# Performance work log

Hardware: AMD Instinct MI355X
Metric: run time of the kernel (lower is better)

The kernel has to match this reference:

```python
import jax, jax.numpy as jnp
import numpy as np
from jax import lax

RULE_START = 85
ALPHA = 0.2
SIGMA = 0.05


def setup_inputs() -> dict:
    key = jax.random.key(0)
    ks = jax.random.split(key, 10)
    T, B, H, NR, NO = 512, 256, 512, 20, 33
    D = RULE_START + NR
    s = lambda fan_in: 1.0 / np.sqrt(fan_in)
    return {
        "x": jax.random.normal(ks[0], (T, B, D), jnp.float32),
        "noise": jax.random.uniform(ks[1], (T, B, H), jnp.float32),
        "Ws_w": jax.random.normal(ks[2], (H, RULE_START), jnp.float32) * s(RULE_START),
        "Ws_b": jax.random.normal(ks[3], (H,), jnp.float32) * s(RULE_START),
        "Wr_w": jax.random.normal(ks[4], (H, NR), jnp.float32) * s(NR),
        "Wrec_w": jax.random.normal(ks[5], (H, H), jnp.float32) * s(H),
        "Wrec_b": jax.random.normal(ks[6], (H,), jnp.float32) * s(H),
        "mask": jnp.ones((H, H), jnp.float32),
        "Wout_w": jax.random.normal(ks[7], (NO, H), jnp.float32) * s(H),
        "Wout_b": jax.random.normal(ks[8], (NO,), jnp.float32) * s(H),
    }


def reference(x, noise, Ws_w, Ws_b, Wr_w, Wrec_w, Wrec_b, mask, Wout_w, Wout_b):
    # x: [T, B, rule_start + n_rule]
    sensory = x[:, :, :RULE_START]
    rule = x[:, :, RULE_START:]
    # input projections, batched over all T*B at once
    rnn_inputs = (jnp.einsum('tbd,hd->tbh', sensory, Ws_w) + Ws_b
                  + jnp.einsum('tbr,hr->tbh', rule, Wr_w))  # [T, B, H]
    masked_w = Wrec_w * mask  # [H, H]
    rec_noise = noise * SIGMA  # [T, B, H]

    h0 = jnp.zeros(rnn_inputs.shape[1:], rnn_inputs.dtype)  # [B, H]

    def step(h, inp):
        inp_t, noise_t = inp
        out = jax.nn.relu(inp_t + noise_t + h @ masked_w.T + Wrec_b)
        h_new = ALPHA * out + (1.0 - ALPHA) * h
        return h_new, h_new

    _, hidden_states = lax.scan(step, h0, (rnn_inputs, rec_noise))  # [T, B, H]
    out = jnp.einsum('tbh,oh->tbo', hidden_states, Wout_w) + Wout_b  # [T, B, n_output]
    return out
```

## Files before the change

kernel.cpp:

```cpp
#include <hip/hip_runtime.h>

#define TT 512
#define BB 256
#define HH 512
#define DD 105
#define RS 85
#define NRULE 20
#define NOUT 33
#define HALF 256

#define NFRAG_REC 512
#define NFRAG_IN  128
#define NFRAG_OUT 48
#define FRAG_IN_OFF  (NFRAG_REC)
#define FRAG_OUT_OFF (NFRAG_REC + NFRAG_IN)
#define NFRAG_TOT (NFRAG_REC + NFRAG_IN + NFRAG_OUT)

#define WP_BYTES    ((size_t)NFRAG_TOT * 1024)

#define PREC_OFF    WP_BYTES
#define PREC_STRIDE ((size_t)32768)
#define POUT_OFF    (PREC_OFF + 32 * PREC_STRIDE)
#define POUT_STRIDE ((size_t)9216)
#define EXCH_BYTES  (32 * PREC_STRIDE + 16 * POUT_STRIDE)

#define BPRE_OFF    WP_BYTES
#define BPRE_BYTES  ((size_t)TT * 16 * 16 * 512 * 2)
#define SNEED       (BPRE_OFF + BPRE_BYTES)

#define RETRY_GUARD 100000

typedef __bf16 bf16x8 __attribute__((ext_vector_type(8)));
typedef float  f32x4  __attribute__((ext_vector_type(4)));
typedef unsigned long long u64;
typedef unsigned short us;

__device__ __forceinline__ us f2bf(float f) {
  unsigned u = __builtin_bit_cast(unsigned, f);
  u += 0x7FFFu + ((u >> 16) & 1u);
  return (us)(u >> 16);
}
__device__ __forceinline__ float bf2f(us v) {
  return __builtin_bit_cast(float, (unsigned)v << 16);
}
__device__ __forceinline__ u64 ld_agent(const u64* p) {
  return __hip_atomic_load(p, __ATOMIC_RELAXED, __HIP_MEMORY_SCOPE_AGENT);
}
__device__ __forceinline__ void st_agent(u64* p, u64 v) {
  __hip_atomic_store(p, v, __ATOMIC_RELAXED, __HIP_MEMORY_SCOPE_AGENT);
}
__device__ __forceinline__ float bfhi(unsigned w) {
  return __builtin_bit_cast(float, w & 0xffff0000u);
}
__device__ __forceinline__ unsigned pkv(float v, unsigned tag) {
  return ((unsigned)f2bf(v) << 16) | tag;
}
__device__ __forceinline__ int tags4_ok(u64 v0, u64 v1, u64 v2, u64 v3, unsigned tag) {
  return (((unsigned)v0 & 0xffffu) == tag) & (((unsigned)(v0 >> 32) & 0xffffu) == tag)
       & (((unsigned)v1 & 0xffffu) == tag) & (((unsigned)(v1 >> 32) & 0xffffu) == tag)
       & (((unsigned)v2 & 0xffffu) == tag) & (((unsigned)(v2 >> 32) & 0xffffu) == tag)
       & (((unsigned)v3 & 0xffffu) == tag) & (((unsigned)(v3 >> 32) & 0xffffu) == tag);
}
__device__ __forceinline__ int tags2_ok(u64 v0, u64 v1, unsigned tag) {
  return (((unsigned)v0 & 0xffffu) == tag) & (((unsigned)(v0 >> 32) & 0xffffu) == tag)
       & (((unsigned)v1 & 0xffffu) == tag) & (((unsigned)(v1 >> 32) & 0xffffu) == tag);
}

__global__ void pack_weights(const float* __restrict__ Ws_w, const float* __restrict__ Wr_w,
                             const float* __restrict__ Wrec_w, const float* __restrict__ mask,
                             const float* __restrict__ Wout_w, us* __restrict__ wp)
{
  int gid = blockIdx.x * blockDim.x + threadIdx.x;
  if (gid >= NFRAG_TOT * 64) return;
  int f = gid >> 6, lane = gid & 63;
  int m16 = lane & 15, kg = lane >> 4;
  float v[8];
  if (f < NFRAG_REC) {
    int mt = f >> 4, kt = f & 15;
    int m = mt * 16 + m16, k0 = kt * 32 + kg * 8;
#pragma unroll
    for (int j = 0; j < 8; ++j) {
      int k = k0 + j;
      v[j] = Wrec_w[m * HH + k] * mask[m * HH + k];
    }
  } else if (f < FRAG_OUT_OFF) {
    int ff = f - FRAG_IN_OFF;
    int mt = ff >> 2, kt = ff & 3;
    int m = mt * 16 + m16, k0 = kt * 32 + kg * 8;
#pragma unroll
    for (int j = 0; j < 8; ++j) {
      int k = k0 + j;
      float val = 0.f;
      if (k < RS) val = Ws_w[m * RS + k];
      else if (k < DD) val = Wr_w[m * NRULE + (k - RS)];
      v[j] = val;
    }
  } else {
    int ff = f - FRAG_OUT_OFF;
    int mt = ff >> 4, kt = ff & 15;
    int m = mt * 16 + m16, k0 = kt * 32 + kg * 8;
#pragma unroll
    for (int j = 0; j < 8; ++j) {
      int k = k0 + j;
      v[j] = (m < NOUT) ? Wout_w[m * HH + k] : 0.f;
    }
  }
  unsigned o[4];
#pragma unroll
  for (int j = 0; j < 4; ++j)
    o[j] = (unsigned)f2bf(v[2 * j]) | ((unsigned)f2bf(v[2 * j + 1]) << 16);
  uint4 st = make_uint4(o[0], o[1], o[2], o[3]);
  *reinterpret_cast<uint4*>(wp + (size_t)f * 512 + lane * 8) = st;
}

__global__ __launch_bounds__(512)
void precompute_pre(const float* __restrict__ x, const float* __restrict__ noise,
                    const float* __restrict__ Ws_b, const float* __restrict__ Wrec_b,
                    const us* __restrict__ wp, us* __restrict__ pre)
{
  __shared__ alignas(16) us x_lds[16 * 128];
  const int t  = blockIdx.x >> 4;
  const int gg = blockIdx.x & 15;
  const int gb = gg * 16;
  const int tid = threadIdx.x;
  const int wv = tid >> 6, lane = tid & 63;
  const int bcol = lane & 15, krow = lane >> 4;
  const int sw = (bcol & 7) << 3;
  const uint4* wp4 = reinterpret_cast<const uint4*>(wp);

  for (int i = tid; i < 16 * 128; i += 512) x_lds[i] = 0;
  __syncthreads();
  if (tid < 420) {
    f32x4 xv = reinterpret_cast<const f32x4*>(x + ((size_t)t * BB + gb) * DD)[tid];
#pragma unroll
    for (int j = 0; j < 4; ++j) {
      int e = tid * 4 + j;
      int b = e / DD, k = e - b * DD;
      x_lds[b * 128 + (k ^ ((b & 7) << 3))] = f2bf(xv[j]);
    }
  }
  __syncthreads();

  us ov[16];
#pragma unroll
  for (int jj = 0; jj < 4; ++jj) {
    int m = wv * 4 + jj;
    f32x4 acc = {0.f, 0.f, 0.f, 0.f};
#pragma unroll
    for (int kx = 0; kx < 4; ++kx) {
      int k0 = kx * 32 + krow * 8;
      bf16x8 xb = __builtin_bit_cast(bf16x8,
          *reinterpret_cast<const uint4*>(&x_lds[bcol * 128 + (k0 ^ sw)]));
      bf16x8 aw = __builtin_bit_cast(bf16x8, wp4[(FRAG_IN_OFF + m * 4 + kx) * 64 + lane]);
      acc = __builtin_amdgcn_mfma_f32_16x16x32_bf16(aw, xb, acc, 0, 0, 0);
    }
    int h0 = m * 16 + krow * 4;
    f32x4 b1 = *reinterpret_cast<const f32x4*>(Ws_b + h0);
    f32x4 b2 = *reinterpret_cast<const f32x4*>(Wrec_b + h0);
    f32x4 nz = *reinterpret_cast<const f32x4*>(noise + ((size_t)t * BB + gb + bcol) * HH + h0);
#pragma unroll
    for (int r = 0; r < 4; ++r)
      ov[jj * 4 + r] = f2bf(acc[r] + b1[r] + b2[r] + 0.05f * nz[r]);
  }
  us* dst = pre + (((size_t)t * 16 + gg) * 512 + tid) * 16;
  *reinterpret_cast<uint4*>(dst)     = *reinterpret_cast<uint4*>(&ov[0]);
  *reinterpret_cast<uint4*>(dst + 8) = *reinterpret_cast<uint4*>(&ov[8]);
}

__global__ __launch_bounds__(512, 2)
void rnn_seq16(unsigned char* __restrict__ ws)
{
  __shared__ alignas(16) us h_lds[2][16 * 512];
  __shared__ alignas(16) us wlds[112 * 512];

  const int tid  = threadIdx.x;
  const int wv   = tid >> 6;
  const int lane = tid & 63;
  const int bcol = lane & 15;
  const int krow = lane >> 4;
  const int g    = blockIdx.x;
  const int sw   = (bcol & 7) << 3;
  const uint4* wp4 = reinterpret_cast<const uint4*>(ws);
  us* pre = (us*)(ws + BPRE_OFF);

  {
    us* hz = &h_lds[0][0];
    for (int i = tid; i < 2 * 16 * 512; i += 512) hz[i] = 0;
  }
  for (int c = tid; c < 112 * 64; c += 512) {
    int fl = c >> 6, l = c & 63;
    int w = fl / 14, kt = fl % 14;
    int mt = 4 * w + 3;
    uint4 v = wp4[(mt * 16 + kt) * 64 + l];
    *reinterpret_cast<uint4*>(&wlds[fl * 512 + l * 8]) = v;
  }

  bf16x8 wreg[3][16];
#pragma unroll
  for (int j = 0; j < 3; ++j)
#pragma unroll
    for (int kt = 0; kt < 16; ++kt)
      wreg[j][kt] = __builtin_bit_cast(bf16x8, wp4[((4 * wv + j) * 16 + kt) * 64 + lane]);
  bf16x8 wx[2];
#pragma unroll
  for (int j = 0; j < 2; ++j)
    wx[j] = __builtin_bit_cast(bf16x8, wp4[((4 * wv + 3) * 16 + 14 + j) * 64 + lane]);

  int h0[4];
#pragma unroll
  for (int j = 0; j < 4; ++j) h0[j] = (4 * wv + j) * 16 + krow * 4;

  __syncthreads();

  const size_t tstride = (size_t)16 * 512 * 16;
  us* pio = pre + ((size_t)g * 512 + tid) * 16;

  uint4 hs[2] = {};

#pragma unroll 1
  for (int t = 0; t < TT; ++t) {
    const int cur = t & 1;
    if (t > 0) {
      us* hout = pio + (size_t)(t - 1) * tstride;
      *reinterpret_cast<uint4*>(hout)     = hs[0];
      *reinterpret_cast<uint4*>(hout + 8) = hs[1];
    }
    uint4 pA[2];
    {
      const us* pn = pio + (size_t)t * tstride;
      pA[0] = *reinterpret_cast<const uint4*>(pn);
      pA[1] = *reinterpret_cast<const uint4*>(pn + 8);
    }

    f32x4 acc[4];
#pragma unroll
    for (int j = 0; j < 4; ++j) acc[j] = f32x4{0.f, 0.f, 0.f, 0.f};
    __builtin_amdgcn_s_setprio(1);
#pragma unroll
    for (int kt = 0; kt < 16; ++kt) {
      bf16x8 hb = __builtin_bit_cast(bf16x8,
          *reinterpret_cast<const uint4*>(&h_lds[cur][bcol * 512 + ((kt * 32 + krow * 8) ^ sw)]));
      acc[0] = __builtin_amdgcn_mfma_f32_16x16x32_bf16(wreg[0][kt], hb, acc[0], 0, 0, 0);
      acc[1] = __builtin_amdgcn_mfma_f32_16x16x32_bf16(wreg[1][kt], hb, acc[1], 0, 0, 0);
      acc[2] = __builtin_amdgcn_mfma_f32_16x16x32_bf16(wreg[2][kt], hb, acc[2], 0, 0, 0);
      bf16x8 wl;
      if (kt < 14)
        wl = __builtin_bit_cast(bf16x8,
            *reinterpret_cast<const uint4*>(&wlds[(wv * 14 + kt) * 512 + lane * 8]));
      else
        wl = wx[kt - 14];
      acc[3] = __builtin_amdgcn_mfma_f32_16x16x32_bf16(wl, hb, acc[3], 0, 0, 0);
    }
    __builtin_amdgcn_s_setprio(0);

    {
      const us* pa = reinterpret_cast<const us*>(pA);
      us* hh = reinterpret_cast<us*>(hs);
#pragma unroll
      for (int j = 0; j < 4; ++j)
#pragma unroll
        for (int r = 0; r < 4; ++r) {
          int s = j * 4 + r;
          float v = acc[j][r] + bf2f(pa[s]);
          v = fmaxf(v, 0.f);
          hh[s] = f2bf(0.2f * v + 0.8f * bf2f(hh[s]));
        }
    }
    {
      const us* hh = reinterpret_cast<const us*>(hs);
#pragma unroll
      for (int j = 0; j < 4; ++j) {
        *reinterpret_cast<ushort4*>(&h_lds[cur ^ 1][bcol * 512 + (h0[j] ^ sw)]) =
            make_ushort4(hh[j * 4], hh[j * 4 + 1], hh[j * 4 + 2], hh[j * 4 + 3]);
      }
    }
    __syncthreads();
  }

  {
    us* hout = pio + (size_t)(TT - 1) * tstride;
    *reinterpret_cast<uint4*>(hout)     = hs[0];
    *reinterpret_cast<uint4*>(hout + 8) = hs[1];
  }
}

__global__ __launch_bounds__(256)
void out_gemm(const us* __restrict__ hid, const us* __restrict__ wp,
              const float* __restrict__ Wout_b, float* __restrict__ out)
{
  __shared__ alignas(16) us t_lds[16 * 512];
  const int tid = threadIdx.x;
  const int wv = tid >> 6, lane = tid & 63;
  const int bcol = lane & 15, krow = lane >> 4;
  const int tg = blockIdx.x;
  const int t = tg >> 4, g = tg & 15;
  const int sw = (bcol & 7) << 3;
  const uint4* wp4 = reinterpret_cast<const uint4*>(wp);

#pragma unroll
  for (int q = 0; q < 2; ++q) {
    int cc = tid + q * 256;
    const us* src = hid + (size_t)tg * 8192 + (size_t)cc * 16;
    uint4 v0 = *reinterpret_cast<const uint4*>(src);
    uint4 v1 = *reinterpret_cast<const uint4*>(src + 8);
    us vs[16];
    *reinterpret_cast<uint4*>(&vs[0]) = v0;
    *reinterpret_cast<uint4*>(&vs[8]) = v1;
    int b = cc & 15, kr = (cc >> 4) & 3;
    int swb = (b & 7) << 3;
#pragma unroll
    for (int jj = 0; jj < 4; ++jj) {
      int m = (cc >> 6) * 4 + jj;
      int h = m * 16 + kr * 4;
      *reinterpret_cast<ushort4*>(&t_lds[b * 512 + (h ^ swb)]) =
          make_ushort4(vs[jj * 4], vs[jj * 4 + 1], vs[jj * 4 + 2], vs[jj * 4 + 3]);
    }
  }
  __syncthreads();
  if (wv < 3) {
    f32x4 po = {0.f, 0.f, 0.f, 0.f};
#pragma unroll
    for (int kt = 0; kt < 16; ++kt) {
      bf16x8 hb = __builtin_bit_cast(bf16x8,
          *reinterpret_cast<const uint4*>(&t_lds[bcol * 512 + ((kt * 32 + krow * 8) ^ sw)]));
      bf16x8 ao = __builtin_bit_cast(bf16x8, wp4[(FRAG_OUT_OFF + wv * 16 + kt) * 64 + lane]);
      po = __builtin_amdgcn_mfma_f32_16x16x32_bf16(ao, hb, po, 0, 0, 0);
    }
#pragma unroll
    for (int r = 0; r < 4; ++r) {
      int o = wv * 16 + krow * 4 + r;
      if (o < NOUT)
        out[((size_t)t * BB + g * 16 + bcol) * NOUT + o] = po[r] + Wout_b[o];
    }
  }
}

__global__ __launch_bounds__(512, 2)
void rnn_fused(const float* __restrict__ x, const float* __restrict__ noise,
               const float* __restrict__ Ws_b, const float* __restrict__ Wrec_b,
               const float* __restrict__ Wout_b, unsigned char* __restrict__ ws,
               float* __restrict__ out)
{
  __shared__ alignas(16) us h_lds[16 * HALF];
  __shared__ alignas(16) us x_lds[2][16 * 128];
  __shared__ alignas(16) us win_lds[64 * 512];
  __shared__ alignas(16) us wout_lds[24 * 512];

  const int tid  = threadIdx.x;
  const int wv   = tid >> 6;
  const int lane = tid & 63;
  const int bcol = lane & 15;
  const int krow = lane >> 4;
  const int bid  = blockIdx.x;
  const int g    = bid & 15;
  const int hf   = bid >> 4;
  const int gb   = g * 16;
  const int hbase = hf * HALF;
  const int sw   = (bcol & 7) << 3;
  const bool outduty = (hf == 0);

  const uint4* wp4 = reinterpret_cast<const uint4*>(ws);
  u64* prec_own = (u64*)(ws + PREC_OFF + (size_t)bid * PREC_STRIDE);
  const u64* prec_par = (const u64*)(ws + PREC_OFF + (size_t)(bid ^ 16) * PREC_STRIDE);
  u64* pout_buf = (u64*)(ws + POUT_OFF + (size_t)g * POUT_STRIDE);

  for (int i = tid; i < 16 * HALF; i += 512) h_lds[i] = 0;
  {
    us* xz = &x_lds[0][0];
    for (int i = tid; i < 2 * 16 * 128; i += 512) xz[i] = 0;
  }
  for (int c = tid; c < 64 * 64; c += 512) {
    int fl = c >> 6, l = c & 63;
    uint4 w = wp4[(FRAG_IN_OFF + hf * 64 + fl) * 64 + l];
    *reinterpret_cast<uint4*>(&win_lds[fl * 512 + l * 8]) = w;
  }
  for (int c = tid; c < 24 * 64; c += 512) {
    int fl = c >> 6, l = c & 63;
    int mt_o = fl >> 3, kto = fl & 7;
    uint4 w = wp4[(FRAG_OUT_OFF + mt_o * 16 + hf * 8 + kto) * 64 + l];
    *reinterpret_cast<uint4*>(&wout_lds[fl * 512 + l * 8]) = w;
  }

  bf16x8 wreg_own[2][8], wreg_par[2][8];
#pragma unroll
  for (int j = 0; j < 2; ++j)
#pragma unroll
    for (int kt = 0; kt < 8; ++kt) {
      wreg_own[j][kt] = __builtin_bit_cast(bf16x8,
          wp4[((hf * 16 + 2 * wv + j) * 16 + (hf * 8 + kt)) * 64 + lane]);
      wreg_par[j][kt] = __builtin_bit_cast(bf16x8,
          wp4[(((1 - hf) * 16 + 2 * wv + j) * 16 + (hf * 8 + kt)) * 64 + lane]);
    }

  float bias_reg[2][4];
#pragma unroll
  for (int j = 0; j < 2; ++j)
#pragma unroll
    for (int r = 0; r < 4; ++r) {
      int h = hbase + (2 * wv + j) * 16 + krow * 4 + r;
      bias_reg[j][r] = Ws_b[h] + Wrec_b[h];
    }
  float woutb[4];
#pragma unroll
  for (int r = 0; r < 4; ++r) {
    int o = wv * 16 + krow * 4 + r;
    woutb[r] = (outduty && wv < 3 && o < NOUT) ? Wout_b[o] : 0.f;
  }

  const int rbase = bcol * 256 + 2 * wv * 16 + krow * 4;
  const int ri = rbase >> 1;
  const int oi = (bcol * 48 + wv * 16 + krow * 4) >> 1;

  float hreg[2][4] = {};
  f32x4 nrA[2], nrB[2];
  f32x4 po_hold = {0.f, 0.f, 0.f, 0.f};

  __syncthreads();

  if (tid < 420) {
    f32x4 xv = reinterpret_cast<const f32x4*>(x + (size_t)gb * DD)[tid];
#pragma unroll
    for (int j = 0; j < 4; ++j) {
      int e = tid * 4 + j;
      int b = e / DD, k = e - b * DD;
      x_lds[0][b * 128 + (k ^ ((b & 7) << 3))] = f2bf(xv[j]);
    }
  }
  {
    const float* nb = noise + ((size_t)gb + bcol) * HH + hbase + krow * 4;
#pragma unroll
    for (int j = 0; j < 2; ++j)
      nrA[j] = *reinterpret_cast<const f32x4*>(nb + (2 * wv + j) * 16);
  }
  __syncthreads();

#pragma unroll 1
  for (int t = 0; t < TT; ++t) {
    const int cur = t & 1;
    const unsigned tag = (unsigned)t;
    u64* prec_slot = prec_own + (size_t)(t & 1) * 2048;
    const u64* precp_slot = prec_par + (size_t)(t & 1) * 2048;
    f32x4 xs = {0.f, 0.f, 0.f, 0.f};
    if (t + 1 < TT) {
      if (tid < 420)
        xs = reinterpret_cast<const f32x4*>(x + ((size_t)(t + 1) * BB + gb) * DD)[tid];
      const float* nb = noise + (((size_t)(t + 1)) * BB + gb + bcol) * HH + hbase + krow * 4;
#pragma unroll
      for (int j = 0; j < 2; ++j)
        nrB[j] = *reinterpret_cast<const f32x4*>(nb + (2 * wv + j) * 16);
    }

    if (t > 0) {
      f32x4 pc0 = {0.f,0.f,0.f,0.f}, pc1 = {0.f,0.f,0.f,0.f};
#pragma unroll
      for (int kto = 0; kto < 8; ++kto) {
        int k0 = kto * 32 + krow * 8;
        bf16x8 hb = __builtin_bit_cast(bf16x8,
            *reinterpret_cast<const uint4*>(&h_lds[bcol * HALF + (k0 ^ sw)]));
        pc0 = __builtin_amdgcn_mfma_f32_16x16x32_bf16(wreg_par[0][kto], hb, pc0, 0, 0, 0);
        pc1 = __builtin_amdgcn_mfma_f32_16x16x32_bf16(wreg_par[1][kto], hb, pc1, 0, 0, 0);
      }
      st_agent(prec_slot + ri,     (u64)pkv(pc0[0], tag) | ((u64)pkv(pc0[1], tag) << 32));
      st_agent(prec_slot + ri + 1, (u64)pkv(pc0[2], tag) | ((u64)pkv(pc0[3], tag) << 32));
      st_agent(prec_slot + ri + 8, (u64)pkv(pc1[0], tag) | ((u64)pkv(pc1[1], tag) << 32));
      st_agent(prec_slot + ri + 9, (u64)pkv(pc1[2], tag) | ((u64)pkv(pc1[3], tag) << 32));
    }

    f32x4 acc[2];
    acc[0] = f32x4{0.f,0.f,0.f,0.f};
    acc[1] = f32x4{0.f,0.f,0.f,0.f};
#pragma unroll
    for (int kto = 0; kto < 8; ++kto) {
      int k0 = kto * 32 + krow * 8;
      bf16x8 hb = __builtin_bit_cast(bf16x8,
          *reinterpret_cast<const uint4*>(&h_lds[bcol * HALF + (k0 ^ sw)]));
      acc[0] = __builtin_amdgcn_mfma_f32_16x16x32_bf16(wreg_own[0][kto], hb, acc[0], 0, 0, 0);
      acc[1] = __builtin_amdgcn_mfma_f32_16x16x32_bf16(wreg_own[1][kto], hb, acc[1], 0, 0, 0);
    }
#pragma unroll
    for (int kx = 0; kx < 4; ++kx) {
      int k0 = kx * 32 + krow * 8;
      bf16x8 xb = __builtin_bit_cast(bf16x8,
          *reinterpret_cast<const uint4*>(&x_lds[cur][bcol * 128 + (k0 ^ sw)]));
#pragma unroll
      for (int j = 0; j < 2; ++j) {
        bf16x8 aw = __builtin_bit_cast(bf16x8,
            *reinterpret_cast<const uint4*>(&win_lds[((2 * wv + j) * 4 + kx) * 512 + lane * 8]));
        acc[j] = __builtin_amdgcn_mfma_f32_16x16x32_bf16(aw, xb, acc[j], 0, 0, 0);
      }
    }

    f32x4 po = {0.f, 0.f, 0.f, 0.f};
    if (t > 0 && wv < 3) {
#pragma unroll
      for (int kto = 0; kto < 8; ++kto) {
        int k0 = kto * 32 + krow * 8;
        bf16x8 hb = __builtin_bit_cast(bf16x8,
            *reinterpret_cast<const uint4*>(&h_lds[bcol * HALF + (k0 ^ sw)]));
        bf16x8 ao = __builtin_bit_cast(bf16x8,
            *reinterpret_cast<const uint4*>(&wout_lds[(wv * 8 + kto) * 512 + lane * 8]));
        po = __builtin_amdgcn_mfma_f32_16x16x32_bf16(ao, hb, po, 0, 0, 0);
      }
    }

    f32x4 pa0 = {0.f,0.f,0.f,0.f}, pa1 = {0.f,0.f,0.f,0.f};
    if (t > 0) {
      u64 v0, v1, v2, v3;
      int guard = RETRY_GUARD;
      for (;;) {
        v0 = ld_agent(precp_slot + ri);
        v1 = ld_agent(precp_slot + ri + 1);
        v2 = ld_agent(precp_slot + ri + 8);
        v3 = ld_agent(precp_slot + ri + 9);
        if (__all(tags4_ok(v0, v1, v2, v3, tag)) || --guard == 0) break;
        __builtin_amdgcn_s_sleep(1);
      }
      pa0[0] = bfhi((unsigned)v0); pa0[1] = bfhi((unsigned)(v0 >> 32));
      pa0[2] = bfhi((unsigned)v1); pa0[3] = bfhi((unsigned)(v1 >> 32));
      pa1[0] = bfhi((unsigned)v2); pa1[1] = bfhi((unsigned)(v2 >> 32));
      pa1[2] = bfhi((unsigned)v3); pa1[3] = bfhi((unsigned)(v3 >> 32));
      if (!outduty && wv < 3) {
        u64* ps = pout_buf + (size_t)(t & 1) * 384;
        st_agent(ps + oi,     (u64)pkv(po[0], tag) | ((u64)pkv(po[1], tag) << 32));
        st_agent(ps + oi + 1, (u64)pkv(po[2], tag) | ((u64)pkv(po[3], tag) << 32));
      }
    }

    __syncthreads();

#pragma unroll
    for (int j = 0; j < 2; ++j) {
      us hsv[4];
      f32x4 pa = j ? pa1 : pa0;
#pragma unroll
      for (int r = 0; r < 4; ++r) {
        float v = acc[j][r] + pa[r] + bias_reg[j][r] + 0.05f * nrA[j][r];
        v = fmaxf(v, 0.f);
        float hn = 0.2f * v + 0.8f * hreg[j][r];
        hreg[j][r] = hn;
        hsv[r] = f2bf(hn);
      }
      int hloc = (2 * wv + j) * 16 + krow * 4;
      *reinterpret_cast<ushort4*>(&h_lds[bcol * HALF + (hloc ^ sw)]) =
          make_ushort4(hsv[0], hsv[1], hsv[2], hsv[3]);
    }
    if (t + 1 < TT && tid < 420) {
#pragma unroll
      for (int j = 0; j < 4; ++j) {
        int e = tid * 4 + j;
        int b = e / DD, k = e - b * DD;
        x_lds[cur ^ 1][b * 128 + (k ^ ((b & 7) << 3))] = f2bf(xs[j]);
      }
    }
#pragma unroll
    for (int j = 0; j < 2; ++j) nrA[j] = nrB[j];

    if (outduty && wv < 3 && t >= 2) {
      const unsigned otag = (unsigned)(t - 1);
      const u64* ps = pout_buf + (size_t)((t - 1) & 1) * 384;
      u64 w0, w1;
      int guard = RETRY_GUARD;
      for (;;) {
        w0 = ld_agent(ps + oi);
        w1 = ld_agent(ps + oi + 1);
        if (__all(tags2_ok(w0, w1, otag)) || --guard == 0) break;
        __builtin_amdgcn_s_sleep(1);
      }
      float pr[4] = { bfhi((unsigned)w0), bfhi((unsigned)(w0 >> 32)),
                      bfhi((unsigned)w1), bfhi((unsigned)(w1 >> 32)) };
#pragma unroll
      for (int r = 0; r < 4; ++r) {
        int o = wv * 16 + krow * 4 + r;
        if (o < NOUT)
          out[((size_t)(t - 2) * BB + gb + bcol) * NOUT + o] = po_hold[r] + pr[r] + woutb[r];
      }
    }
    if (outduty && wv < 3 && t > 0) po_hold = po;

    __syncthreads();
  }

  if (!outduty && wv < 3) {
    f32x4 po = {0.f, 0.f, 0.f, 0.f};
#pragma unroll
    for (int kto = 0; kto < 8; ++kto) {
      int k0 = kto * 32 + krow * 8;
      bf16x8 hb = __builtin_bit_cast(bf16x8,
          *reinterpret_cast<const uint4*>(&h_lds[bcol * HALF + (k0 ^ sw)]));
      bf16x8 ao = __builtin_bit_cast(bf16x8,
          *reinterpret_cast<const uint4*>(&wout_lds[(wv * 8 + kto) * 512 + lane * 8]));
      po = __builtin_amdgcn_mfma_f32_16x16x32_bf16(ao, hb, po, 0, 0, 0);
    }
    const unsigned tagT = (unsigned)TT;
    u64* ps = pout_buf + (size_t)2 * 384;
    st_agent(ps + oi,     (u64)pkv(po[0], tagT) | ((u64)pkv(po[1], tagT) << 32));
    st_agent(ps + oi + 1, (u64)pkv(po[2], tagT) | ((u64)pkv(po[3], tagT) << 32));
  }
  if (outduty && wv < 3) {
    {
      const unsigned otag = (unsigned)(TT - 1);
      const u64* ps = pout_buf + (size_t)((TT - 1) & 1) * 384;
      u64 w0, w1;
      int guard = RETRY_GUARD;
      for (;;) {
        w0 = ld_agent(ps + oi);
        w1 = ld_agent(ps + oi + 1);
        if (__all(tags2_ok(w0, w1, otag)) || --guard == 0) break;
        __builtin_amdgcn_s_sleep(1);
      }
      float pr[4] = { bfhi((unsigned)w0), bfhi((unsigned)(w0 >> 32)),
                      bfhi((unsigned)w1), bfhi((unsigned)(w1 >> 32)) };
#pragma unroll
      for (int r = 0; r < 4; ++r) {
        int o = wv * 16 + krow * 4 + r;
        if (o < NOUT)
          out[((size_t)(TT - 2) * BB + gb + bcol) * NOUT + o] = po_hold[r] + pr[r] + woutb[r];
      }
    }
    {
      f32x4 po = {0.f, 0.f, 0.f, 0.f};
#pragma unroll
      for (int kto = 0; kto < 8; ++kto) {
        int k0 = kto * 32 + krow * 8;
        bf16x8 hb = __builtin_bit_cast(bf16x8,
            *reinterpret_cast<const uint4*>(&h_lds[bcol * HALF + (k0 ^ sw)]));
        bf16x8 ao = __builtin_bit_cast(bf16x8,
            *reinterpret_cast<const uint4*>(&wout_lds[(wv * 8 + kto) * 512 + lane * 8]));
        po = __builtin_amdgcn_mfma_f32_16x16x32_bf16(ao, hb, po, 0, 0, 0);
      }
      const unsigned tagT = (unsigned)TT;
      const u64* ps = pout_buf + (size_t)2 * 384;
      u64 w0, w1;
      int guard = RETRY_GUARD;
      for (;;) {
        w0 = ld_agent(ps + oi);
        w1 = ld_agent(ps + oi + 1);
        if (__all(tags2_ok(w0, w1, tagT)) || --guard == 0) break;
        __builtin_amdgcn_s_sleep(1);
      }
      float pr[4] = { bfhi((unsigned)w0), bfhi((unsigned)(w0 >> 32)),
                      bfhi((unsigned)w1), bfhi((unsigned)(w1 >> 32)) };
#pragma unroll
      for (int r = 0; r < 4; ++r) {
        int o = wv * 16 + krow * 4 + r;
        if (o < NOUT)
          out[((size_t)(TT - 1) * BB + gb + bcol) * NOUT + o] = po[r] + pr[r] + woutb[r];
      }
    }
  }
}

extern "C" void kernel_launch(void* const* d_in, const int* in_sizes, int n_in,
                              void* d_out, int out_size, void* d_ws, size_t ws_size,
                              hipStream_t stream) {
  (void)in_sizes; (void)n_in; (void)out_size;
  const float* x      = (const float*)d_in[0];
  const float* noise  = (const float*)d_in[1];
  const float* Ws_w   = (const float*)d_in[2];
  const float* Ws_b   = (const float*)d_in[3];
  const float* Wr_w   = (const float*)d_in[4];
  const float* Wrec_w = (const float*)d_in[5];
  const float* Wrec_b = (const float*)d_in[6];
  const float* mask   = (const float*)d_in[7];
  const float* Wout_w = (const float*)d_in[8];
  const float* Wout_b = (const float*)d_in[9];
  unsigned char* ws   = (unsigned char*)d_ws;
  float* out          = (float*)d_out;

  pack_weights<<<(NFRAG_TOT * 64 + 255) / 256, 256, 0, stream>>>(
      Ws_w, Wr_w, Wrec_w, mask, Wout_w, (us*)ws);

  if (ws_size >= (size_t)SNEED) {
    us* pre = (us*)(ws + BPRE_OFF);
    precompute_pre<<<TT * 16, 512, 0, stream>>>(x, noise, Ws_b, Wrec_b, (us*)ws, pre);
    rnn_seq16<<<16, 512, 0, stream>>>(ws);
    out_gemm<<<TT * 16, 256, 0, stream>>>(pre, (us*)ws, Wout_b, out);
  } else {
    hipMemsetAsync(ws + PREC_OFF, 0, EXCH_BYTES, stream);
    rnn_fused<<<32, 512, 0, stream>>>(x, noise, Ws_b, Wrec_b, Wout_b, ws, out);
  }
}
```

Measured before the change: 1.704 ms.

## Rebalance recurrent weight storage across registers, LDS and per-step global loads

Each wave now keeps only two row tiles of the recurrent weights in registers. A third tile mostly moves to LDS (15 k-tiles, up from 14), and the fourth tile is re-read from global or L2 every step in two batches of eight. The h reads from LDS are batched into register arrays in two halves ahead of the MFMA loops. The hidden state is now carried in fp32 registers instead of being rounded to bf16 every step, and uses the native bf16 conversion. The aim is to free VGPRs and raise overlap, at the price of extra global traffic per step inside the latency-bound recurrence.

```diff
diff --git a/kernel.cpp b/kernel.cpp
--- a/kernel.cpp
+++ b/kernel.cpp
@@ -51,6 +51,9 @@
 }
 __device__ __forceinline__ float bfhi(unsigned w) {
   return __builtin_bit_cast(float, w & 0xffff0000u);
+}
+__device__ __forceinline__ float bflo(unsigned w) {
+  return __builtin_bit_cast(float, w << 16);
 }
 __device__ __forceinline__ unsigned pkv(float v, unsigned tag) {
   return ((unsigned)f2bf(v) << 16) | tag;
@@ -171,7 +174,7 @@
 void rnn_seq16(unsigned char* __restrict__ ws)
 {
   __shared__ alignas(16) us h_lds[2][16 * 512];
-  __shared__ alignas(16) us wlds[112 * 512];
+  __shared__ alignas(16) us wlds[120 * 512];
 
   const int tid  = threadIdx.x;
   const int wv   = tid >> 6;
@@ -187,24 +190,22 @@
     us* hz = &h_lds[0][0];
     for (int i = tid; i < 2 * 16 * 512; i += 512) hz[i] = 0;
   }
-  for (int c = tid; c < 112 * 64; c += 512) {
+  for (int c = tid; c < 120 * 64; c += 512) {
     int fl = c >> 6, l = c & 63;
-    int w = fl / 14, kt = fl % 14;
-    int mt = 4 * w + 3;
-    uint4 v = wp4[(mt * 16 + kt) * 64 + l];
+    int w = fl / 15, kt = fl % 15;
+    uint4 v = wp4[((4 * w + 2) * 16 + kt) * 64 + l];
     *reinterpret_cast<uint4*>(&wlds[fl * 512 + l * 8]) = v;
   }
 
-  bf16x8 wreg[3][16];
-#pragma unroll
-  for (int j = 0; j < 3; ++j)
+  bf16x8 wreg[2][16];
+#pragma unroll
+  for (int j = 0; j < 2; ++j)
 #pragma unroll
     for (int kt = 0; kt < 16; ++kt)
       wreg[j][kt] = __builtin_bit_cast(bf16x8, wp4[((4 * wv + j) * 16 + kt) * 64 + lane]);
-  bf16x8 wx[2];
-#pragma unroll
-  for (int j = 0; j < 2; ++j)
-    wx[j] = __builtin_bit_cast(bf16x8, wp4[((4 * wv + 3) * 16 + 14 + j) * 64 + lane]);
+
+  const uint4* wgp  = wp4 + (size_t)((4 * wv + 3) * 16) * 64 + lane;
+  const uint4* wg2p = wp4 + (size_t)((4 * wv + 2) * 16 + 15) * 64 + lane;
 
   int h0[4];
 #pragma unroll
@@ -215,59 +216,105 @@
   const size_t tstride = (size_t)16 * 512 * 16;
   us* pio = pre + ((size_t)g * 512 + tid) * 16;
 
-  uint4 hs[2] = {};
+  float hf[16];
+#pragma unroll
+  for (int s = 0; s < 16; ++s) hf[s] = 0.f;
+  uint4 hsw[2];
+  hsw[0] = make_uint4(0, 0, 0, 0);
+  hsw[1] = make_uint4(0, 0, 0, 0);
 
 #pragma unroll 1
   for (int t = 0; t < TT; ++t) {
     const int cur = t & 1;
     if (t > 0) {
       us* hout = pio + (size_t)(t - 1) * tstride;
-      *reinterpret_cast<uint4*>(hout)     = hs[0];
-      *reinterpret_cast<uint4*>(hout + 8) = hs[1];
-    }
-    uint4 pA[2];
+      *reinterpret_cast<uint4*>(hout)     = hsw[0];
+      *reinterpret_cast<uint4*>(hout + 8) = hsw[1];
+    }
+    uint4 pA0, pA1;
     {
       const us* pn = pio + (size_t)t * tstride;
-      pA[0] = *reinterpret_cast<const uint4*>(pn);
-      pA[1] = *reinterpret_cast<const uint4*>(pn + 8);
-    }
+      pA0 = *reinterpret_cast<const uint4*>(pn);
+      pA1 = *reinterpret_cast<const uint4*>(pn + 8);
+    }
+    uint4 wg[8];
+#pragma unroll
+    for (int q = 0; q < 8; ++q) wg[q] = wgp[q * 64];
 
     f32x4 acc[4];
 #pragma unroll
     for (int j = 0; j < 4; ++j) acc[j] = f32x4{0.f, 0.f, 0.f, 0.f};
+
+    uint4 hbr[8];
+#pragma unroll
+    for (int q = 0; q < 8; ++q)
+      hbr[q] = *reinterpret_cast<const uint4*>(
+          &h_lds[cur][bcol * 512 + ((q * 32 + krow * 8) ^ sw)]);
     __builtin_amdgcn_s_setprio(1);
 #pragma unroll
-    for (int kt = 0; kt < 16; ++kt) {
-      bf16x8 hb = __builtin_bit_cast(bf16x8,
-          *reinterpret_cast<const uint4*>(&h_lds[cur][bcol * 512 + ((kt * 32 + krow * 8) ^ sw)]));
+    for (int kt = 0; kt < 8; ++kt) {
+      bf16x8 hb = __builtin_bit_cast(bf16x8, hbr[kt]);
       acc[0] = __builtin_amdgcn_mfma_f32_16x16x32_bf16(wreg[0][kt], hb, acc[0], 0, 0, 0);
       acc[1] = __builtin_amdgcn_mfma_f32_16x16x32_bf16(wreg[1][kt], hb, acc[1], 0, 0, 0);
-      acc[2] = __builtin_amdgcn_mfma_f32_16x16x32_bf16(wreg[2][kt], hb, acc[2], 0, 0, 0);
+      bf16x8 wl = __builtin_bit_cast(bf16x8,
+          *reinterpret_cast<const uint4*>(&wlds[(wv * 15 + kt) * 512 + lane * 8]));
+      acc[2] = __builtin_amdgcn_mfma_f32_16x16x32_bf16(wl, hb, acc[2], 0, 0, 0);
+      acc[3] = __builtin_amdgcn_mfma_f32_16x16x32_bf16(
+          __builtin_bit_cast(bf16x8, wg[kt]), hb, acc[3], 0, 0, 0);
+    }
+    __builtin_amdgcn_s_setprio(0);
+#pragma unroll
+    for (int q = 0; q < 8; ++q) wg[q] = wgp[(8 + q) * 64];
+    uint4 wgx = wg2p[0];
+#pragma unroll
+    for (int q = 0; q < 8; ++q)
+      hbr[q] = *reinterpret_cast<const uint4*>(
+          &h_lds[cur][bcol * 512 + (((8 + q) * 32 + krow * 8) ^ sw)]);
+    __builtin_amdgcn_s_setprio(1);
+#pragma unroll
+    for (int kt = 8; kt < 16; ++kt) {
+      bf16x8 hb = __builtin_bit_cast(bf16x8, hbr[kt - 8]);
+      acc[0] = __builtin_amdgcn_mfma_f32_16x16x32_bf16(wreg[0][kt], hb, acc[0], 0, 0, 0);
+      acc[1] = __builtin_amdgcn_mfma_f32_16x16x32_bf16(wreg[1][kt], hb, acc[1], 0, 0, 0);
       bf16x8 wl;
-      if (kt < 14)
+      if (kt < 15)
         wl = __builtin_bit_cast(bf16x8,
-            *reinterpret_cast<const uint4*>(&wlds[(wv * 14 + kt) * 512 + lane * 8]));
+            *reinterpret_cast<const uint4*>(&wlds[(wv * 15 + kt) * 512 + lane * 8]));
       else
-        wl = wx[kt - 14];
-      acc[3] = __builtin_amdgcn_mfma_f32_16x16x32_bf16(wl, hb, acc[3], 0, 0, 0);
+        wl = __builtin_bit_cast(bf16x8, wgx);
+      acc[2] = __builtin_amdgcn_mfma_f32_16x16x32_bf16(wl, hb, acc[2], 0, 0, 0);
+      acc[3] = __builtin_amdgcn_mfma_f32_16x16x32_bf16(
+          __builtin_bit_cast(bf16x8, wg[kt - 8]), hb, acc[3], 0, 0, 0);
     }
     __builtin_amdgcn_s_setprio(0);
 
     {
-      const us* pa = reinterpret_cast<const us*>(pA);
-      us* hh = reinterpret_cast<us*>(hs);
-#pragma unroll
-      for (int j = 0; j < 4; ++j)
-#pragma unroll
-        for (int r = 0; r < 4; ++r) {
-          int s = j * 4 + r;
-          float v = acc[j][r] + bf2f(pa[s]);
-          v = fmaxf(v, 0.f);
-          hh[s] = f2bf(0.2f * v + 0.8f * bf2f(hh[s]));
+      const unsigned* paw = reinterpret_cast<const unsigned*>(&pA0);
+      unsigned pw[8];
+      *reinterpret_cast<uint4*>(&pw[0]) = pA0;
+      *reinterpret_cast<uint4*>(&pw[4]) = pA1;
+      (void)paw;
+      unsigned* hw = reinterpret_cast<unsigned*>(&hsw[0]);
+#pragma unroll
+      for (int j = 0; j < 4; ++j) {
+#pragma unroll
+        for (int p = 0; p < 2; ++p) {
+          unsigned w = pw[j * 2 + p];
+          float p0 = bflo(w), p1 = bfhi(w);
+          int s0 = j * 4 + p * 2;
+          float v0 = fmaxf(acc[j][p * 2]     + p0, 0.f);
+          float v1 = fmaxf(acc[j][p * 2 + 1] + p1, 0.f);
+          hf[s0]     = 0.2f * v0 + 0.8f * hf[s0];
+          hf[s0 + 1] = 0.2f * v1 + 0.8f * hf[s0 + 1];
+          __bf16 b0 = (__bf16)hf[s0];
+          __bf16 b1 = (__bf16)hf[s0 + 1];
+          hw[j * 2 + p] = (unsigned)__builtin_bit_cast(us, b0)
+                        | ((unsigned)__builtin_bit_cast(us, b1) << 16);
         }
+      }
     }
     {
-      const us* hh = reinterpret_cast<const us*>(hs);
+      const us* hh = reinterpret_cast<const us*>(&hsw[0]);
 #pragma unroll
       for (int j = 0; j < 4; ++j) {
         *reinterpret_cast<ushort4*>(&h_lds[cur ^ 1][bcol * 512 + (h0[j] ^ sw)]) =
@@ -279,8 +326,8 @@
 
   {
     us* hout = pio + (size_t)(TT - 1) * tstride;
-    *reinterpret_cast<uint4*>(hout)     = hs[0];
-    *reinterpret_cast<uint4*>(hout + 8) = hs[1];
+    *reinterpret_cast<uint4*>(hout)     = hsw[0];
+    *reinterpret_cast<uint4*>(hout + 8) = hsw[1];
   }
 }
 
```

Result: slower. 2.412 ms (+41.6%).
